# Kernel tuning notes

Measured on AMD Instinct MI355X. Metric: run time of the kernel, lower is better.

Reference implementation:

```python
import jax, jax.numpy as jnp
import numpy as np

# Winograd F(4x4, 5x5) transform matrices (input tile 8x8)
AT_NP = np.array([
    [1.0, 1.0, 1.0, 1.0, 1.0, 8.0, 8.0, 0.0],
    [0.0, 1.0, -1.0, 2.0, -2.0, 4.0, -4.0, 0.0],
    [0.0, 1.0, 1.0, 4.0, 4.0, 2.0, 2.0, 0.0],
    [0.0, 1.0, -1.0, 8.0, -8.0, 1.0, -1.0, 1.0]], dtype=np.float32)

BT_NP = np.array([
    [1.0, 0.0, -21.0/4.0, 0.0, 21.0/4.0, 0.0, -1.0, 0.0],
    [0.0, 1.0, 1.0, -17.0/4.0, -17.0/4.0, 1.0, 1.0, 0.0],
    [0.0, -1.0, 1.0, 17.0/4.0, -17.0/4.0, -1.0, 1.0, 0.0],
    [0.0, 0.5, 0.25, -2.5, -1.25, 2.0, 1.0, 0.0],
    [0.0, -0.5, 0.25, 2.5, -1.25, -2.0, 1.0, 0.0],
    [0.0, 2.0, 4.0, -2.5, -5.0, 0.5, 1.0, 0.0],
    [0.0, -2.0, 4.0, 2.5, -5.0, -0.5, 1.0, 0.0],
    [0.0, -1.0, 0.0, 21.0/4.0, 0.0, -21.0/4.0, 0.0, 1.0]], dtype=np.float32)

N, IC, OC, HW = 8, 128, 128, 68  # output spatial = 68-5+1 = 64, tiles 16x16


def setup_inputs() -> dict:
    key = jax.random.key(0)
    k1, k2, k3 = jax.random.split(key, 3)
    x = jax.random.normal(k1, (N, IC, HW, HW), dtype=jnp.float32)
    # weight is stored in the Winograd (transformed) domain: [OC, IC, 8, 8]
    weight = jax.random.normal(k2, (OC, IC, 8, 8), dtype=jnp.float32) * 0.02
    bias = 1.0 + 0.01 * jax.random.normal(k3, (OC,), dtype=jnp.float32)
    return {"x": x, "weight": weight, "bias": bias}


def reference(x, weight, bias):
    BT = jnp.asarray(BT_NP)
    AT = jnp.asarray(AT_NP)
    n, c, H, W = x.shape
    oc = weight.shape[0]
    tH = (H - 8) // 4 + 1
    tW = (W - 8) // 4 + 1
    # extract overlapping 8x8 tiles with stride 4 (torch unfold)
    ih = (jnp.arange(tH) * 4)[:, None] + jnp.arange(8)  # [tH, 8]
    iw = (jnp.arange(tW) * 4)[:, None] + jnp.arange(8)  # [tW, 8]
    tiles = x[:, :, ih, :]            # [n, c, tH, 8, W]
    tiles = tiles[:, :, :, :, iw]     # [n, c, tH, 8, tW, 8]
    tiles = tiles.transpose(0, 1, 2, 4, 3, 5)  # [n, c, tH, tW, 8, 8]
    # input transform: BT @ d @ B
    xt = jnp.einsum('ai,nchwij,bj->nchwab', BT, tiles, BT)
    # channel reduction with elementwise 8x8 multiply (Winograd domain)
    yt = jnp.einsum('nchwab,ocab->nohwab', xt, weight)
    # output transform: AT @ m @ A -> [n, oc, tH, tW, 4, 4]
    y = jnp.einsum('pa,nohwab,qb->nohwpq', AT, yt, AT)
    y = y.transpose(0, 1, 2, 4, 3, 5).reshape(n, oc, tH * 4, tW * 4)
    return y + bias[None, :, None, None]
```

## Files before the change

### kernel.cpp

```cpp
#include <hip/hip_runtime.h>

#define N_    8
#define IC_   128
#define OC_   128
#define HW_   68
#define M_    2048
#define OW_   64

constexpr float BT[8][8] = {
  {1.f, 0.f, -5.25f, 0.f, 5.25f, 0.f, -1.f, 0.f},
  {0.f, 1.f, 1.f, -4.25f, -4.25f, 1.f, 1.f, 0.f},
  {0.f, -1.f, 1.f, 4.25f, -4.25f, -1.f, 1.f, 0.f},
  {0.f, 0.5f, 0.25f, -2.5f, -1.25f, 2.f, 1.f, 0.f},
  {0.f, -0.5f, 0.25f, 2.5f, -1.25f, -2.f, 1.f, 0.f},
  {0.f, 2.f, 4.f, -2.5f, -5.f, 0.5f, 1.f, 0.f},
  {0.f, -2.f, 4.f, 2.5f, -5.f, -0.5f, 1.f, 0.f},
  {0.f, -1.f, 0.f, 5.25f, 0.f, -5.25f, 0.f, 1.f}
};
constexpr float AT[4][8] = {
  {1.f, 1.f, 1.f, 1.f, 1.f, 8.f, 8.f, 0.f},
  {0.f, 1.f, -1.f, 2.f, -2.f, 4.f, -4.f, 0.f},
  {0.f, 1.f, 1.f, 4.f, 4.f, 2.f, 2.f, 0.f},
  {0.f, 1.f, -1.f, 8.f, -8.f, 1.f, -1.f, 1.f}
};

__device__ __forceinline__ float bf2f(unsigned short u) {
  union { unsigned int i; float f; } v; v.i = ((unsigned int)u) << 16; return v.f;
}
__device__ __forceinline__ unsigned short f2bf(float f) {
  union { float f; unsigned int i; } v; v.f = f;
  unsigned int r = v.i + 0x7FFFu + ((v.i >> 16) & 1u);
  return (unsigned short)(r >> 16);
}

typedef __attribute__((ext_vector_type(8))) short short8;
typedef __attribute__((ext_vector_type(4))) float f32x4;

#define K1_CPITCH 580
__global__ __launch_bounds__(512) void k_in_wt(const float* __restrict__ x,
                                               const float* __restrict__ w,
                                               unsigned short* __restrict__ xt,
                                               unsigned short* __restrict__ wT) {
  const int cg = blockIdx.x, th = blockIdx.y, n = blockIdx.z;
  const int tid = threadIdx.x;

  if (th == 16) {
    const int wb = n * 4 + cg;
    const int gtid = wb * 512 + tid;
    for (int g = gtid; g < 262144; g += 16384) {
      const int ab4 = g & 15;
      const int c  = (g >> 4) & 127;
      const int oc = g >> 11;
      const float4 v = *reinterpret_cast<const float4*>(
          w + ((size_t)(oc * 128 + c)) * 64 + ab4 * 4);
      const float vv[4] = {v.x, v.y, v.z, v.w};
#pragma unroll
      for (int k = 0; k < 4; ++k)
        wT[(size_t)(ab4 * 4 + k) * 16384 + oc * 128 + c] = f2bf(vv[k]);
    }
    return;
  }

  const int c0 = cg * 32;
  const int h0 = th * 4;
  __shared__ unsigned short xs[32 * K1_CPITCH];

  for (int idx = tid; idx < 32 * 8 * 17; idx += 512) {
    const int ci = idx / 136;
    const int rem = idx - ci * 136;
    const int r = rem / 17;
    const int f = rem - r * 17;
    const float4 v = *reinterpret_cast<const float4*>(
        x + ((size_t)((n * IC_ + c0 + ci) * HW_ + h0 + r)) * HW_ + f * 4);
    ushort4 s;
    s.x = f2bf(v.x); s.y = f2bf(v.y); s.z = f2bf(v.z); s.w = f2bf(v.w);
    *reinterpret_cast<ushort4*>(&xs[ci * K1_CPITCH + r * 72 + f * 4]) = s;
  }
  __syncthreads();

  const int ct = tid & 31;
  const int tw = tid >> 5;
  const unsigned short* xp = &xs[ct * K1_CPITCH];

  float t1[8][8];
#pragma unroll
  for (int a = 0; a < 8; ++a)
#pragma unroll
    for (int j = 0; j < 8; ++j) t1[a][j] = 0.f;

#pragma unroll
  for (int i = 0; i < 8; ++i) {
    const ushort4 u0 = *reinterpret_cast<const ushort4*>(xp + i * 72 + tw * 4);
    const ushort4 u1 = *reinterpret_cast<const ushort4*>(xp + i * 72 + tw * 4 + 4);
    const float r8[8] = {bf2f(u0.x), bf2f(u0.y), bf2f(u0.z), bf2f(u0.w),
                         bf2f(u1.x), bf2f(u1.y), bf2f(u1.z), bf2f(u1.w)};
#pragma unroll
    for (int a = 0; a < 8; ++a) {
      const float ba = BT[a][i];
      if (ba != 0.f) {
#pragma unroll
        for (int j = 0; j < 8; ++j) t1[a][j] += ba * r8[j];
      }
    }
  }

  const int m = n * 256 + th * 16 + tw;
  const size_t base = (size_t)m * 128 + c0 + ct;
#pragma unroll
  for (int a = 0; a < 8; ++a) {
#pragma unroll
    for (int b = 0; b < 8; ++b) {
      float v = 0.f;
#pragma unroll
      for (int j = 0; j < 8; ++j) {
        const float bb = BT[b][j];
        if (bb != 0.f) v += t1[a][j] * bb;
      }
      xt[(size_t)(a * 8 + b) * (M_ * 128) + base] = f2bf(v);
    }
  }
}

__global__ __launch_bounds__(512) void k_gemm(const unsigned short* __restrict__ xt,
                                              const unsigned short* __restrict__ wT,
                                              unsigned short* __restrict__ yt) {
  const int ab = blockIdx.z;
  const int m0 = blockIdx.x * 128;
  const unsigned short* Ag = xt + (size_t)ab * (M_ * 128);
  const unsigned short* Bg = wT + (size_t)ab * (128 * 128);
  unsigned short* Cg = yt + (size_t)ab * (M_ * 128);

  __shared__ unsigned short As[128 * 128];
  __shared__ unsigned short Bs[128 * 128];

  const int tid = threadIdx.x;
  const int lane = tid & 63;
  const int wv = tid >> 6;

#pragma unroll
  for (int i = 0; i < 4; ++i) {
    const int inst = wv * 4 + i;
    const int r = inst * 4 + (lane >> 4);
    const int j = (lane & 15) ^ (r & 7);
    __builtin_amdgcn_global_load_lds(
        (const __attribute__((address_space(1))) void*)(Ag + (size_t)(m0 + r) * 128 + j * 8),
        (__attribute__((address_space(3))) void*)(As + inst * 512), 16, 0, 0);
  }
#pragma unroll
  for (int i = 0; i < 4; ++i) {
    const int inst = wv * 4 + i;
    const int r = inst * 4 + (lane >> 4);
    const int j = (lane & 15) ^ (r & 7);
    __builtin_amdgcn_global_load_lds(
        (const __attribute__((address_space(1))) void*)(Bg + (size_t)r * 128 + j * 8),
        (__attribute__((address_space(3))) void*)(Bs + inst * 512), 16, 0, 0);
  }
  __syncthreads();

  const int wm = wv >> 1, wn = wv & 1;
  const int m_base = wm * 32;
  const int oc_base = wn * 64;
  const int lr = lane & 15;
  const int lg = lane >> 4;

  f32x4 acc[2][4];
#pragma unroll
  for (int mi = 0; mi < 2; ++mi)
#pragma unroll
    for (int ni = 0; ni < 4; ++ni) acc[mi][ni] = (f32x4){0.f, 0.f, 0.f, 0.f};

#pragma unroll
  for (int kk = 0; kk < 4; ++kk) {
    short8 af[2], bf[4];
#pragma unroll
    for (int mi = 0; mi < 2; ++mi) {
      const int row = m_base + mi * 16 + lr;
      const int chunk = (kk * 4 + lg) ^ (row & 7);
      af[mi] = *reinterpret_cast<const short8*>(&As[row * 128 + chunk * 8]);
    }
#pragma unroll
    for (int ni = 0; ni < 4; ++ni) {
      const int row = oc_base + ni * 16 + lr;
      const int chunk = (kk * 4 + lg) ^ (row & 7);
      bf[ni] = *reinterpret_cast<const short8*>(&Bs[row * 128 + chunk * 8]);
    }
#pragma unroll
    for (int mi = 0; mi < 2; ++mi)
#pragma unroll
      for (int ni = 0; ni < 4; ++ni)
        acc[mi][ni] = __builtin_amdgcn_mfma_f32_16x16x32_bf16(af[mi], bf[ni], acc[mi][ni], 0, 0, 0);
  }

#pragma unroll
  for (int mi = 0; mi < 2; ++mi) {
#pragma unroll
    for (int ni = 0; ni < 4; ++ni) {
#pragma unroll
      for (int j = 0; j < 4; ++j) {
        const int row = m0 + m_base + mi * 16 + lg * 4 + j;
        const int col = oc_base + ni * 16 + lr;
        Cg[(size_t)row * 128 + col] = f2bf(acc[mi][ni][j]);
      }
    }
  }
}

__global__ __launch_bounds__(512) void k_output_tf(const unsigned short* __restrict__ yt,
                                                   const float* __restrict__ bias,
                                                   float* __restrict__ y) {
  const int og = blockIdx.x;
  const int thw = blockIdx.y;
  const int n = blockIdx.z;
  const int oc0 = og * 64;
  const int tid = threadIdx.x;
  const int ocl = tid & 63;
  const int tw = tid >> 6;
  const int m = n * 256 + thw * 8 + tw;
  const int th = thw >> 1;
  const int wq = thw & 1;

  __shared__ float ys[64 * 128];

  float Y[8][8];
  const size_t rb = (size_t)m * 128 + oc0 + ocl;
#pragma unroll
  for (int a = 0; a < 8; ++a)
#pragma unroll
    for (int b = 0; b < 8; ++b)
      Y[a][b] = bf2f(yt[(size_t)(a * 8 + b) * (M_ * 128) + rb]);

  float t2[4][8];
#pragma unroll
  for (int p = 0; p < 4; ++p)
#pragma unroll
    for (int b = 0; b < 8; ++b) {
      float v = 0.f;
#pragma unroll
      for (int a = 0; a < 8; ++a) {
        const float aa = AT[p][a];
        if (aa != 0.f) v += aa * Y[a][b];
      }
      t2[p][b] = v;
    }

  const float bv = bias[oc0 + ocl];
#pragma unroll
  for (int p = 0; p < 4; ++p) {
    float o[4];
#pragma unroll
    for (int q = 0; q < 4; ++q) {
      float v = 0.f;
#pragma unroll
      for (int b = 0; b < 8; ++b) {
        const float ab_ = AT[q][b];
        if (ab_ != 0.f) v += t2[p][b] * ab_;
      }
      o[q] = v + bv;
    }
    const float4 ov = {o[0], o[1], o[2], o[3]};
    *reinterpret_cast<float4*>(&ys[ocl * 128 + p * 32 + ((tw ^ (ocl & 7)) * 4)]) = ov;
  }
  __syncthreads();

#pragma unroll
  for (int it = 0; it < 4; ++it) {
    const int idx = it * 512 + tid;
    const int f = idx & 7;
    const int p = (idx >> 3) & 3;
    const int row = idx >> 5;
    const float4 v = *reinterpret_cast<const float4*>(
        &ys[row * 128 + p * 32 + ((f ^ (row & 7)) * 4)]);
    *reinterpret_cast<float4*>(
        y + (((size_t)(n * OC_ + oc0 + row) * OW_) + th * 4 + p) * OW_ + wq * 32 + f * 4) = v;
  }
}

extern "C" void kernel_launch(void* const* d_in, const int* in_sizes, int n_in,
                              void* d_out, int out_size, void* d_ws, size_t ws_size,
                              hipStream_t stream) {
  (void)in_sizes; (void)n_in; (void)out_size; (void)ws_size;
  const float* x    = (const float*)d_in[0];
  const float* w    = (const float*)d_in[1];
  const float* bias = (const float*)d_in[2];
  float* y = (float*)d_out;

  char* ws = (char*)d_ws;
  unsigned short* xt = (unsigned short*)ws;
  unsigned short* yt = (unsigned short*)(ws + (size_t)32 * 1024 * 1024);
  unsigned short* wT = (unsigned short*)(ws + (size_t)64 * 1024 * 1024);

  hipLaunchKernelGGL(k_in_wt, dim3(4, 17, 8), dim3(512), 0, stream, x, w, xt, wT);
  hipLaunchKernelGGL(k_gemm, dim3(16, 1, 64), dim3(512), 0, stream, xt, wT, yt);
  hipLaunchKernelGGL(k_output_tf, dim3(2, 32, 8), dim3(512), 0, stream, yt, bias, y);
}
```

Baseline: 119.7 us.

## Fuse first output-transform stage into batched GEMM epilogue

The GEMM kernel now loops over the 8 'a' indices for a fixed 'b' and accumulates AT[p][a]-weighted results in registers. It writes only 4x8 intermediate planes instead of 8x8, which halves the bf16 intermediate written and read by the output kernel. The output kernel now reads these planes directly and applies only the second transform. In exchange, each GEMM block loops sequentially over 8 K-tiles with two barriers per step and no double buffering. The grid shrinks from 1024 blocks to 256 with a 64-row M tile.

```diff
diff --git a/kernel.cpp b/kernel.cpp
--- a/kernel.cpp
+++ b/kernel.cpp
@@ -121,93 +121,109 @@
   }
 }
 
-__global__ __launch_bounds__(512) void k_gemm(const unsigned short* __restrict__ xt,
-                                              const unsigned short* __restrict__ wT,
-                                              unsigned short* __restrict__ yt) {
-  const int ab = blockIdx.z;
-  const int m0 = blockIdx.x * 128;
-  const unsigned short* Ag = xt + (size_t)ab * (M_ * 128);
-  const unsigned short* Bg = wT + (size_t)ab * (128 * 128);
-  unsigned short* Cg = yt + (size_t)ab * (M_ * 128);
-
-  __shared__ unsigned short As[128 * 128];
+__global__ __launch_bounds__(512) void k_gemm_z(const unsigned short* __restrict__ xt,
+                                                const unsigned short* __restrict__ wT,
+                                                unsigned short* __restrict__ Z) {
+  const int b  = blockIdx.y;
+  const int m0 = blockIdx.x * 64;
+
+  __shared__ unsigned short As[64 * 128];
   __shared__ unsigned short Bs[128 * 128];
 
   const int tid = threadIdx.x;
   const int lane = tid & 63;
   const int wv = tid >> 6;
-
-#pragma unroll
-  for (int i = 0; i < 4; ++i) {
-    const int inst = wv * 4 + i;
-    const int r = inst * 4 + (lane >> 4);
-    const int j = (lane & 15) ^ (r & 7);
-    __builtin_amdgcn_global_load_lds(
-        (const __attribute__((address_space(1))) void*)(Ag + (size_t)(m0 + r) * 128 + j * 8),
-        (__attribute__((address_space(3))) void*)(As + inst * 512), 16, 0, 0);
-  }
-#pragma unroll
-  for (int i = 0; i < 4; ++i) {
-    const int inst = wv * 4 + i;
-    const int r = inst * 4 + (lane >> 4);
-    const int j = (lane & 15) ^ (r & 7);
-    __builtin_amdgcn_global_load_lds(
-        (const __attribute__((address_space(1))) void*)(Bg + (size_t)r * 128 + j * 8),
-        (__attribute__((address_space(3))) void*)(Bs + inst * 512), 16, 0, 0);
-  }
-  __syncthreads();
-
-  const int wm = wv >> 1, wn = wv & 1;
-  const int m_base = wm * 32;
-  const int oc_base = wn * 64;
   const int lr = lane & 15;
   const int lg = lane >> 4;
-
-  f32x4 acc[2][4];
-#pragma unroll
-  for (int mi = 0; mi < 2; ++mi)
-#pragma unroll
-    for (int ni = 0; ni < 4; ++ni) acc[mi][ni] = (f32x4){0.f, 0.f, 0.f, 0.f};
-
-#pragma unroll
-  for (int kk = 0; kk < 4; ++kk) {
-    short8 af[2], bf[4];
-#pragma unroll
-    for (int mi = 0; mi < 2; ++mi) {
-      const int row = m_base + mi * 16 + lr;
-      const int chunk = (kk * 4 + lg) ^ (row & 7);
-      af[mi] = *reinterpret_cast<const short8*>(&As[row * 128 + chunk * 8]);
-    }
+  const int wm = wv >> 1, wn = wv & 1;
+  const int m_base = wm * 16;
+  const int oc_base = wn * 64;
+
+  f32x4 zacc[4][4];
+#pragma unroll
+  for (int p = 0; p < 4; ++p)
+#pragma unroll
+    for (int ni = 0; ni < 4; ++ni) zacc[p][ni] = (f32x4){0.f, 0.f, 0.f, 0.f};
+
+#pragma unroll
+  for (int a = 0; a < 8; ++a) {
+    const int ab = a * 8 + b;
+    const unsigned short* Ag = xt + (size_t)ab * (M_ * 128) + (size_t)m0 * 128;
+    const unsigned short* Bg = wT + (size_t)ab * 16384;
+
+#pragma unroll
+    for (int i = 0; i < 2; ++i) {
+      const int inst = wv * 2 + i;
+      const int r = inst * 4 + lg;
+      const int j = lr ^ (r & 7);
+      __builtin_amdgcn_global_load_lds(
+          (const __attribute__((address_space(1))) void*)(Ag + (size_t)r * 128 + j * 8),
+          (__attribute__((address_space(3))) void*)(As + inst * 512), 16, 0, 0);
+    }
+#pragma unroll
+    for (int i = 0; i < 4; ++i) {
+      const int inst = wv * 4 + i;
+      const int r = inst * 4 + lg;
+      const int j = lr ^ (r & 7);
+      __builtin_amdgcn_global_load_lds(
+          (const __attribute__((address_space(1))) void*)(Bg + (size_t)r * 128 + j * 8),
+          (__attribute__((address_space(3))) void*)(Bs + inst * 512), 16, 0, 0);
+    }
+    __syncthreads();
+
+    f32x4 acc[4];
+#pragma unroll
+    for (int ni = 0; ni < 4; ++ni) acc[ni] = (f32x4){0.f, 0.f, 0.f, 0.f};
+
+#pragma unroll
+    for (int kk = 0; kk < 4; ++kk) {
+      const int arow = m_base + lr;
+      const short8 af = *reinterpret_cast<const short8*>(
+          &As[arow * 128 + ((kk * 4 + lg) ^ (arow & 7)) * 8]);
+      short8 bf[4];
+#pragma unroll
+      for (int ni = 0; ni < 4; ++ni) {
+        const int brow = oc_base + ni * 16 + lr;
+        bf[ni] = *reinterpret_cast<const short8*>(
+            &Bs[brow * 128 + ((kk * 4 + lg) ^ (brow & 7)) * 8]);
+      }
+#pragma unroll
+      for (int ni = 0; ni < 4; ++ni)
+        acc[ni] = __builtin_amdgcn_mfma_f32_16x16x32_bf16(af, bf[ni], acc[ni], 0, 0, 0);
+    }
+
+#pragma unroll
+    for (int p = 0; p < 4; ++p) {
+      const float w_ = AT[p][a];
+      if (w_ != 0.f) {
+#pragma unroll
+        for (int ni = 0; ni < 4; ++ni)
+#pragma unroll
+          for (int j = 0; j < 4; ++j)
+            zacc[p][ni][j] += w_ * acc[ni][j];
+      }
+    }
+    __syncthreads();
+  }
+
+#pragma unroll
+  for (int p = 0; p < 4; ++p) {
+    unsigned short* Zp = Z + (size_t)(p * 8 + b) * (M_ * 128);
 #pragma unroll
     for (int ni = 0; ni < 4; ++ni) {
-      const int row = oc_base + ni * 16 + lr;
-      const int chunk = (kk * 4 + lg) ^ (row & 7);
-      bf[ni] = *reinterpret_cast<const short8*>(&Bs[row * 128 + chunk * 8]);
-    }
-#pragma unroll
-    for (int mi = 0; mi < 2; ++mi)
-#pragma unroll
-      for (int ni = 0; ni < 4; ++ni)
-        acc[mi][ni] = __builtin_amdgcn_mfma_f32_16x16x32_bf16(af[mi], bf[ni], acc[mi][ni], 0, 0, 0);
-  }
-
-#pragma unroll
-  for (int mi = 0; mi < 2; ++mi) {
-#pragma unroll
-    for (int ni = 0; ni < 4; ++ni) {
 #pragma unroll
       for (int j = 0; j < 4; ++j) {
-        const int row = m0 + m_base + mi * 16 + lg * 4 + j;
+        const int row = m0 + m_base + lg * 4 + j;
         const int col = oc_base + ni * 16 + lr;
-        Cg[(size_t)row * 128 + col] = f2bf(acc[mi][ni][j]);
-      }
-    }
-  }
-}
-
-__global__ __launch_bounds__(512) void k_output_tf(const unsigned short* __restrict__ yt,
-                                                   const float* __restrict__ bias,
-                                                   float* __restrict__ y) {
+        Zp[(size_t)row * 128 + col] = f2bf(zacc[p][ni][j]);
+      }
+    }
+  }
+}
+
+__global__ __launch_bounds__(512) void k_output_z(const unsigned short* __restrict__ Z,
+                                                  const float* __restrict__ bias,
+                                                  float* __restrict__ y) {
   const int og = blockIdx.x;
   const int thw = blockIdx.y;
   const int n = blockIdx.z;
@@ -221,27 +237,13 @@
 
   __shared__ float ys[64 * 128];
 
-  float Y[8][8];
+  float t2[4][8];
   const size_t rb = (size_t)m * 128 + oc0 + ocl;
 #pragma unroll
-  for (int a = 0; a < 8; ++a)
+  for (int p = 0; p < 4; ++p)
 #pragma unroll
     for (int b = 0; b < 8; ++b)
-      Y[a][b] = bf2f(yt[(size_t)(a * 8 + b) * (M_ * 128) + rb]);
-
-  float t2[4][8];
-#pragma unroll
-  for (int p = 0; p < 4; ++p)
-#pragma unroll
-    for (int b = 0; b < 8; ++b) {
-      float v = 0.f;
-#pragma unroll
-      for (int a = 0; a < 8; ++a) {
-        const float aa = AT[p][a];
-        if (aa != 0.f) v += aa * Y[a][b];
-      }
-      t2[p][b] = v;
-    }
+      t2[p][b] = bf2f(Z[(size_t)(p * 8 + b) * (M_ * 128) + rb]);
 
   const float bv = bias[oc0 + ocl];
 #pragma unroll
@@ -286,10 +288,10 @@
 
   char* ws = (char*)d_ws;
   unsigned short* xt = (unsigned short*)ws;
-  unsigned short* yt = (unsigned short*)(ws + (size_t)32 * 1024 * 1024);
+  unsigned short* Zb = (unsigned short*)(ws + (size_t)32 * 1024 * 1024);
   unsigned short* wT = (unsigned short*)(ws + (size_t)64 * 1024 * 1024);
 
   hipLaunchKernelGGL(k_in_wt, dim3(4, 17, 8), dim3(512), 0, stream, x, w, xt, wT);
-  hipLaunchKernelGGL(k_gemm, dim3(16, 1, 64), dim3(512), 0, stream, xt, wT, yt);
-  hipLaunchKernelGGL(k_output_tf, dim3(2, 32, 8), dim3(512), 0, stream, yt, bias, y);
-}
+  hipLaunchKernelGGL(k_gemm_z, dim3(32, 8), dim3(512), 0, stream, xt, wT, Zb);
+  hipLaunchKernelGGL(k_output_z, dim3(2, 32, 8), dim3(512), 0, stream, Zb, bias, y);
+}
```

Result: no change. 119.6 us (-0.2%).
